# Performance work log

Hardware: AMD Instinct MI355X
Metric: run time of the kernel (lower is better)

Reference implementation:

```python
import jax, jax.numpy as jnp
import numpy as np

DIM, DH, H_HEADS, F, HH, WW = 512, 64, 8, 16, 32, 32
FF_IN = int(DIM * 4 * 2 / 3)  # 1365


def _ln(x, w, b):
    m = x.mean(-1, keepdims=True)
    v = ((x - m) ** 2).mean(-1, keepdims=True)
    return (x - m) * jax.lax.rsqrt(v + 1e-5) * w + b


def _attn(x, ln_w, ln_b, wq, wkv, nkv, nbias, wout, oln_w, oln_b, rel_bias):
    # x: (B, N, D); K/V are single-head (shared across heads) per the source to_kv
    B, N, D = x.shape
    H = nbias.shape[0]
    dh = nkv.shape[-1]
    xn = _ln(x, ln_w, ln_b)
    q = (xn @ wq).reshape(B, N, H, dh).transpose(0, 2, 1, 3) * (dh ** -0.5)
    k, v = jnp.split(xn @ wkv, 2, axis=-1)  # (B, N, dh) each
    nk = jnp.broadcast_to(nkv[0], (B, 1, dh))
    nv = jnp.broadcast_to(nkv[1], (B, 1, dh))
    k = jnp.concatenate([nk, k], axis=1)  # (B, N+1, dh)
    v = jnp.concatenate([nv, v], axis=1)
    sim = jnp.einsum('bhid,bjd->bhij', q, k)  # (B, H, N, N+1)
    bias = jnp.concatenate([jnp.broadcast_to(nbias[:, None, None], (H, N, 1)), rel_bias], axis=-1)
    attn = jax.nn.softmax(sim + bias[None], axis=-1)
    out = jnp.einsum('bhij,bjd->bhid', attn, v)
    out = out.transpose(0, 2, 1, 3).reshape(B, N, H * dh)
    return _ln(out @ wout, oln_w, oln_b)


def _cpb_mlp(coords, w0, b0, w1, b1, w2, b2):
    t = jax.nn.silu(coords @ w0 + b0)
    t = jax.nn.silu(t @ w1 + b1)
    return t @ w2 + b2  # (R, heads)


def _spatial_bias(h, w, w0, b0, w1, b1, w2, b2):
    rh = jnp.arange(-h + 1, h)
    rw = jnp.arange(-w + 1, w)
    gh, gw = jnp.meshgrid(rh, rw, indexing='ij')
    coords = jnp.stack([gh, gw], axis=-1).reshape(-1, 2).astype(jnp.float32)
    table = _cpb_mlp(coords, w0, b0, w1, b1, w2, b2)  # ((2h-1)(2w-1), H)
    ph, pw = jnp.meshgrid(jnp.arange(h), jnp.arange(w), indexing='ij')
    p = jnp.stack([ph, pw], axis=-1).reshape(-1, 2)  # (hw, 2)
    rel = p[:, None] - p[None]  # (hw, hw, 2)
    idx = (rel[..., 0] + h - 1) * (2 * w - 1) + (rel[..., 1] + w - 1)
    return table[idx].transpose(2, 0, 1)  # (H, hw, hw)


def _temporal_bias(f, w0, b0, w1, b1, w2, b2):
    coords = jnp.arange(-f + 1, f, dtype=jnp.float32)[:, None]
    table = _cpb_mlp(coords, w0, b0, w1, b1, w2, b2)  # (2f-1, H)
    idx = jnp.arange(f)[:, None] - jnp.arange(f)[None] + f - 1
    return table[idx].transpose(2, 0, 1)  # (H, f, f)


def _ff(x, win, g, wout):
    # 1x1x1 conv == channel matmul; GEGLU; shift_token; ChanLayerNorm; conv out
    y = jnp.einsum('bcfhw,cd->bdfhw', x, win)
    a, gate = jnp.split(y, 2, axis=1)
    y = a * jax.nn.gelu(gate, approximate=False)
    c = y.shape[1]
    c1 = (c + 1) // 2  # torch.chunk: first chunk gets ceil
    y1, y2 = y[:, :c1], y[:, c1:]
    y2 = jnp.pad(y2, ((0, 0), (0, 0), (1, 0), (0, 0), (0, 0)))[:, :, :-1]
    y = jnp.concatenate([y1, y2], axis=1)
    m = y.mean(1, keepdims=True)
    v = ((y - m) ** 2).mean(1, keepdims=True)
    y = (y - m) * jax.lax.rsqrt(jnp.maximum(v, 1e-5)) * g.reshape(1, -1, 1, 1, 1)
    return jnp.einsum('bcfhw,cd->bdfhw', y, wout)


def setup_inputs() -> dict:
    key = jax.random.key(0)
    ks = jax.random.split(key, 32)
    d2 = DIM // 2
    inner = DH * H_HEADS

    def nrm(k, shape, s=0.02):
        return jax.random.normal(k, shape, jnp.float32) * s

    inp = {'x': jax.random.normal(ks[0], (1, DIM, F, HH, WW), jnp.float32)}
    for pre, i in (('sa', 1), ('ta', 11)):
        inp[pre + '_ln_w'] = jnp.ones(DIM, jnp.float32)
        inp[pre + '_ln_b'] = jnp.zeros(DIM, jnp.float32)
        inp[pre + '_wq'] = nrm(ks[i], (DIM, inner))
        inp[pre + '_wkv'] = nrm(ks[i + 1], (DIM, 2 * DH))
        inp[pre + '_null_kv'] = nrm(ks[i + 2], (2, DH), 1.0)
        inp[pre + '_null_bias'] = nrm(ks[i + 3], (H_HEADS,), 1.0)
        inp[pre + '_wout'] = nrm(ks[i + 4], (inner, DIM))
        inp[pre + '_oln_w'] = jnp.ones(DIM, jnp.float32)
        inp[pre + '_oln_b'] = jnp.zeros(DIM, jnp.float32)
    inp['sp_w0'] = nrm(ks[20], (2, d2), 0.1); inp['sp_b0'] = jnp.zeros(d2, jnp.float32)
    inp['sp_w1'] = nrm(ks[21], (d2, d2), 0.05); inp['sp_b1'] = jnp.zeros(d2, jnp.float32)
    inp['sp_w2'] = nrm(ks[22], (d2, H_HEADS), 0.05); inp['sp_b2'] = jnp.zeros(H_HEADS, jnp.float32)
    inp['tp_w0'] = nrm(ks[23], (1, d2), 0.1); inp['tp_b0'] = jnp.zeros(d2, jnp.float32)
    inp['tp_w1'] = nrm(ks[24], (d2, d2), 0.05); inp['tp_b1'] = jnp.zeros(d2, jnp.float32)
    inp['tp_w2'] = nrm(ks[25], (d2, H_HEADS), 0.05); inp['tp_b2'] = jnp.zeros(H_HEADS, jnp.float32)
    inp['ff_win'] = nrm(ks[26], (DIM, 2 * FF_IN))
    inp['ff_g'] = jnp.ones(FF_IN, jnp.float32)
    inp['ff_wout'] = nrm(ks[27], (FF_IN, DIM))
    return inp


def _forward(x, sa_ln_w, sa_ln_b, sa_wq, sa_wkv, sa_null_kv, sa_null_bias, sa_wout, sa_oln_w, sa_oln_b,
             ta_ln_w, ta_ln_b, ta_wq, ta_wkv, ta_null_kv, ta_null_bias, ta_wout, ta_oln_w, ta_oln_b,
             sp_w0, sp_b0, sp_w1, sp_b1, sp_w2, sp_b2,
             tp_w0, tp_b0, tp_w1, tp_b1, tp_w2, tp_b2,
             ff_win, ff_g, ff_wout):
    b, c, f, h, w = x.shape
    # spatial attention over (h*w) tokens, batched over (b*f)
    xs = x.transpose(0, 2, 3, 4, 1).reshape(b * f, h * w, c)
    sb = _spatial_bias(h, w, sp_w0, sp_b0, sp_w1, sp_b1, sp_w2, sp_b2)
    xs = _attn(xs, sa_ln_w, sa_ln_b, sa_wq, sa_wkv, sa_null_kv, sa_null_bias, sa_wout, sa_oln_w, sa_oln_b, sb) + xs
    xv = xs.reshape(b, f, h, w, c).transpose(0, 4, 1, 2, 3)
    # temporal attention over f tokens, batched over (b*h*w)
    xt = xv.transpose(0, 3, 4, 2, 1).reshape(b * h * w, f, c)
    tb = _temporal_bias(f, tp_w0, tp_b0, tp_w1, tp_b1, tp_w2, tp_b2)
    xt = _attn(xt, ta_ln_w, ta_ln_b, ta_wq, ta_wkv, ta_null_kv, ta_null_bias, ta_wout, ta_oln_w, ta_oln_b, tb) + xt
    xv = xt.reshape(b, h, w, f, c).transpose(0, 4, 3, 1, 2)
    # feed-forward with token shift
    return _ff(xv, ff_win, ff_g, ff_wout) + xv


def reference(x, sa_ln_w, sa_ln_b, sa_wq, sa_wkv, sa_null_kv, sa_null_bias, sa_wout, sa_oln_w, sa_oln_b,
              ta_ln_w, ta_ln_b, ta_wq, ta_wkv, ta_null_kv, ta_null_bias, ta_wout, ta_oln_w, ta_oln_b,
              sp_w0, sp_b0, sp_w1, sp_b1, sp_w2, sp_b2,
              tp_w0, tp_b0, tp_w1, tp_b1, tp_w2, tp_b2,
              ff_win, ff_g, ff_wout):
    return _forward(x, sa_ln_w, sa_ln_b, sa_wq, sa_wkv, sa_null_kv, sa_null_bias, sa_wout, sa_oln_w, sa_oln_b,
                    ta_ln_w, ta_ln_b, ta_wq, ta_wkv, ta_null_kv, ta_null_bias, ta_wout, ta_oln_w, ta_oln_b,
                    sp_w0, sp_b0, sp_w1, sp_b1, sp_w2, sp_b2,
                    tp_w0, tp_b0, tp_w1, tp_b1, tp_w2, tp_b2,
                    ff_win, ff_g, ff_wout)
```

## Files before the change

### kernel.cpp

```cpp
#include <hip/hip_runtime.h>
#include <math.h>

#define TOK 16384
#define DIMC 512
#define FFI 1365
#define CH1 683
#define YSLD 1376
#define KVPAD 1056
#define BSTRIDE 1152
#define MASKB (-30000.f)
#define LOG2E 1.4426950408889634f

typedef unsigned int u32;
typedef unsigned short ushort_t;
typedef __attribute__((ext_vector_type(8))) short bf16x8;
typedef __attribute__((ext_vector_type(4))) float f32x4;

__device__ inline ushort_t f2b(float x) {
    u32 u = __float_as_uint(x);
    u32 r = (u + 0x7fffu + ((u >> 16) & 1u)) >> 16;
    return (ushort_t)r;
}
__device__ inline float b2f(ushort_t u) { return __uint_as_float(((u32)u) << 16); }

__device__ inline float exp2_fast(float x) {
    float r;
    asm("v_exp_f32 %0, %1" : "=v"(r) : "v"(x));
    return r;
}

__device__ inline u32 cvt_pk_bf16(float lo, float hi) {
    u32 r;
    asm("v_cvt_pk_bf16_f32 %0, %1, %2" : "=v"(r) : "v"(lo), "v"(hi));
    return r;
}

__device__ inline void gload_lds16(const void* g, void* l) {
    __builtin_amdgcn_global_load_lds(
        (const __attribute__((address_space(1))) u32*)g,
        (__attribute__((address_space(3))) u32*)l, 16, 0, 0);
}

__device__ inline float gelu_exact(float x) {
    return 0.5f * x * (1.f + erff(x * 0.70710678118654752f));
}

__device__ inline void waitcnt_vm4() {
    asm volatile("s_waitcnt vmcnt(4)" ::: "memory");
    __builtin_amdgcn_sched_barrier(0);
}
__device__ inline void waitcnt_vm0() {
    asm volatile("s_waitcnt vmcnt(0)" ::: "memory");
    __builtin_amdgcn_sched_barrier(0);
}

__global__ __launch_bounds__(256) void cpb_kernel(
    const float* __restrict__ w0, const float* __restrict__ b0,
    const float* __restrict__ w1, const float* __restrict__ b1,
    const float* __restrict__ w2, const float* __restrict__ b2,
    float* __restrict__ table, int mode, int nrows)
{
    __shared__ float t0[16][256];
    __shared__ float t1[16][256];
    int r0 = blockIdx.x * 16;
    int t = threadIdx.x;
    float w0t = w0[t], b0t = b0[t];
    float w0t2 = (mode == 0) ? w0[256 + t] : 0.f;
    #pragma unroll
    for (int rr = 0; rr < 16; ++rr) {
        int r = r0 + rr; if (r >= nrows) r = nrows - 1;
        float c0, c1;
        if (mode == 0) { c0 = (float)(r / 63 - 31); c1 = (float)(r % 63 - 31); }
        else           { c0 = (float)(r - 15);      c1 = 0.f; }
        float a = c0 * w0t + b0t;
        if (mode == 0) a += c1 * w0t2;
        t0[rr][t] = a / (1.f + __expf(-a));
    }
    __syncthreads();
    float b1t = b1[t];
    float acc[16];
    #pragma unroll
    for (int rr = 0; rr < 16; ++rr) acc[rr] = b1t;
    for (int k = 0; k < 256; ++k) {
        float w = w1[k * 256 + t];
        #pragma unroll
        for (int rr = 0; rr < 16; ++rr) acc[rr] += t0[rr][k] * w;
    }
    #pragma unroll
    for (int rr = 0; rr < 16; ++rr) {
        float s = acc[rr];
        t1[rr][t] = s / (1.f + __expf(-s));
    }
    __syncthreads();
    if (t < 128) {
        int rr = t >> 3, oo = t & 7;
        int r = r0 + rr;
        if (r < nrows) {
            float o = b2[oo];
            for (int k = 0; k < 256; ++k) o += t1[rr][k] * w2[k * 8 + oo];
            table[r * 8 + oo] = o;
        }
    }
}

__global__ __launch_bounds__(256) void bias_sp_kernel(
    const float* __restrict__ tab, const float* __restrict__ nullbias,
    ushort_t* __restrict__ out)
{
    int pi = blockIdx.x, h = blockIdx.y;
    int phi = pi >> 5, pwi = pi & 31;
    ushort_t* row = out + ((size_t)h * 1024 + pi) * BSTRIDE;
    for (int c = threadIdx.x; c < BSTRIDE; c += 256) {
        float v;
        if (c == 0) v = nullbias[h];
        else if (c <= 1024) {
            int pj = c - 1;
            int phj = pj >> 5, pwj = pj & 31;
            int idx = (phi - phj + 31) * 63 + (pwi - pwj + 31);
            v = tab[idx * 8 + h];
        } else v = MASKB;
        row[c] = f2b(v * LOG2E);
    }
}

__global__ __launch_bounds__(256) void kvinit_kernel(
    const float* __restrict__ nullkv, ushort_t* __restrict__ KP, ushort_t* __restrict__ VT)
{
    int f = blockIdx.x, t = threadIdx.x;
    for (int e = t; e < 32 * 64; e += 256) {
        int rr = e >> 6, d = e & 63;
        int row = (rr == 0) ? 0 : (1024 + rr);
        KP[((size_t)f * KVPAD + row) * 64 + d] = (rr == 0) ? f2b(nullkv[d]) : (ushort_t)0;
    }
    for (int e = t; e < 64 * 32; e += 256) {
        int d = e >> 5, cc = e & 31;
        int col = (cc == 0) ? 0 : (1024 + cc);
        VT[((size_t)f * 64 + d) * KVPAD + col] = (cc == 0) ? f2b(nullkv[64 + d]) : (ushort_t)0;
    }
}

__global__ __launch_bounds__(256) void wcvt_kernel(
    const float* __restrict__ W, int ldw, int c0,
    ushort_t* __restrict__ Bt, int Kp, int K, int Ncols,
    const float* __restrict__ gv, int Nwrite)
{
    __shared__ float tile[32][33];
    int nb = blockIdx.x * 32, kb = blockIdx.y * 32;
    int tx = threadIdx.x & 31, ty = threadIdx.x >> 5;
    #pragma unroll
    for (int it = 0; it < 4; ++it) {
        int k = kb + ty + it * 8, n = nb + tx;
        float v = (k < K && n < Ncols) ? W[(size_t)k * ldw + c0 + n] : 0.f;
        if (gv && k < K) v *= gv[k];
        tile[ty + it * 8][tx] = v;
    }
    __syncthreads();
    #pragma unroll
    for (int it = 0; it < 4; ++it) {
        int n = nb + ty + it * 8, k = kb + tx;
        if (n < Nwrite && k < Kp) Bt[(size_t)n * Kp + k] = f2b(tile[tx][ty + it * 8]);
    }
}

__global__ __launch_bounds__(256) void transpose_in_kernel(
    const float* __restrict__ x, float* __restrict__ dst)
{
    __shared__ float tile[32][33];
    int t0b = blockIdx.x * 32, c0b = blockIdx.y * 32;
    int tx = threadIdx.x & 31, ty = threadIdx.x >> 5;
    #pragma unroll
    for (int it = 0; it < 4; ++it) {
        int c = ty + it * 8;
        tile[c][tx] = x[(size_t)(c0b + c) * TOK + t0b + tx];
    }
    __syncthreads();
    #pragma unroll
    for (int it = 0; it < 4; ++it) {
        int tr = ty + it * 8;
        dst[(size_t)(t0b + tr) * DIMC + c0b + tx] = tile[tx][tr];
    }
}

__global__ __launch_bounds__(256) void ln_bf16_kernel(
    const float* __restrict__ in, ushort_t* __restrict__ out,
    const float* __restrict__ w, const float* __restrict__ b)
{
    __shared__ float r1[4], r2[4];
    size_t base = (size_t)blockIdx.x * DIMC;
    int t = threadIdx.x;
    float x0 = in[base + t], x1 = in[base + 256 + t];
    float s = x0 + x1, s2 = x0 * x0 + x1 * x1;
    #pragma unroll
    for (int o = 32; o > 0; o >>= 1) { s += __shfl_down(s, o, 64); s2 += __shfl_down(s2, o, 64); }
    if ((t & 63) == 0) { r1[t >> 6] = s; r2[t >> 6] = s2; }
    __syncthreads();
    float mean = (r1[0] + r1[1] + r1[2] + r1[3]) * (1.f / 512.f);
    float ex2  = (r2[0] + r2[1] + r2[2] + r2[3]) * (1.f / 512.f);
    float rstd = rsqrtf(ex2 - mean * mean + 1e-5f);
    out[base + t]       = f2b((x0 - mean) * rstd * w[t] + b[t]);
    out[base + 256 + t] = f2b((x1 - mean) * rstd * w[256 + t] + b[256 + t]);
}

__global__ __launch_bounds__(256) void ln_add_kernel(
    const float* __restrict__ proj, float* __restrict__ io,
    const float* __restrict__ w, const float* __restrict__ b)
{
    __shared__ float r1[4], r2[4];
    size_t base = (size_t)blockIdx.x * DIMC;
    int t = threadIdx.x;
    float x0 = proj[base + t], x1 = proj[base + 256 + t];
    float s = x0 + x1, s2 = x0 * x0 + x1 * x1;
    #pragma unroll
    for (int o = 32; o > 0; o >>= 1) { s += __shfl_down(s, o, 64); s2 += __shfl_down(s2, o, 64); }
    if ((t & 63) == 0) { r1[t >> 6] = s; r2[t >> 6] = s2; }
    __syncthreads();
    float mean = (r1[0] + r1[1] + r1[2] + r1[3]) * (1.f / 512.f);
    float ex2  = (r2[0] + r2[1] + r2[2] + r2[3]) * (1.f / 512.f);
    float rstd = rsqrtf(ex2 - mean * mean + 1e-5f);
    io[base + t]       += (x0 - mean) * rstd * w[t] + b[t];
    io[base + 256 + t] += (x1 - mean) * rstd * w[256 + t] + b[256 + t];
}

__global__ __launch_bounds__(128) void permute0_kernel(
    const float* __restrict__ src, float* __restrict__ dst)
{
    int rd = blockIdx.x;
    int rs = (rd & 15) * 1024 + (rd >> 4);
    ((float4*)(dst + (size_t)rd * DIMC))[threadIdx.x] =
        ((const float4*)(src + (size_t)rs * DIMC))[threadIdx.x];
}

__global__ __launch_bounds__(128) void permute1_dual_kernel(
    const float* __restrict__ src, float* __restrict__ dst, ushort_t* __restrict__ dstb)
{
    int rd = blockIdx.x;
    int rs = (rd & 1023) * 16 + (rd >> 10);
    float4 v = ((const float4*)(src + (size_t)rs * DIMC))[threadIdx.x];
    ((float4*)(dst + (size_t)rd * DIMC))[threadIdx.x] = v;
    u32 lo = (u32)f2b(v.x) | ((u32)f2b(v.y) << 16);
    u32 hi = (u32)f2b(v.z) | ((u32)f2b(v.w) << 16);
    ((uint2*)(dstb + (size_t)rd * DIMC))[threadIdx.x] = make_uint2(lo, hi);
}

template<int EPI>
__global__ __launch_bounds__(256) void gemm_mfma(
    const ushort_t* __restrict__ A, int lda,
    const ushort_t* __restrict__ Bt, int Kp,
    float* __restrict__ C, ushort_t* __restrict__ Cb, int ldc,
    int M, int N, int K, float scale, int nx,
    const float* __restrict__ stats, const float* __restrict__ g,
    const float* __restrict__ resid, float* __restrict__ outT,
    ushort_t* __restrict__ KPo, ushort_t* __restrict__ VTo)
{
    __shared__ __align__(16) ushort_t As[2][4 * 128 * 8];
    __shared__ __align__(16) ushort_t Bs[2][4 * 128 * 8];
    int lin = blockIdx.x;
    int xcd = lin & 7, idx = lin >> 3;
    int m0 = (xcd * 16 + (idx & 15)) * 128;
    int n0 = (idx >> 4) * 128;
    int tid = threadIdx.x, lane = tid & 63, wid = tid >> 6;
    int wy = wid >> 1, wx = wid & 1, quad = lane >> 4, l16 = lane & 15;
    bool bfull = (n0 + 128 <= N);
    f32x4 acc[4][4];
    #pragma unroll
    for (int i = 0; i < 4; ++i)
        #pragma unroll
        for (int j = 0; j < 4; ++j) { acc[i][j][0]=0.f; acc[i][j][1]=0.f; acc[i][j][2]=0.f; acc[i][j][3]=0.f; }

    if (bfull) {
        int NT = K >> 5;
        int c0 = wid * 128 + lane, c1 = wid * 128 + 64 + lane;
        const ushort_t* gA0 = A + (size_t)(m0 + (c0 & 127)) * lda + (c0 >> 7) * 8;
        const ushort_t* gA1 = A + (size_t)(m0 + (c1 & 127)) * lda + (c1 >> 7) * 8;
        const ushort_t* gB0 = Bt + (size_t)(n0 + (c0 & 127)) * Kp + (c0 >> 7) * 8;
        const ushort_t* gB1 = Bt + (size_t)(n0 + (c1 & 127)) * Kp + (c1 >> 7) * 8;
        const int lo0 = (wid * 128) * 8, lo1 = (wid * 128 + 64) * 8;
        auto stage = [&](int buf) {
            gload_lds16(gA0, &As[buf][lo0]);
            gload_lds16(gA1, &As[buf][lo1]);
            gload_lds16(gB0, &Bs[buf][lo0]);
            gload_lds16(gB1, &Bs[buf][lo1]);
            gA0 += 32; gA1 += 32; gB0 += 32; gB1 += 32;
        };
        stage(0);
        if (NT > 1) stage(1);
        for (int t = 0; t < NT; ++t) {
            if (t + 1 < NT) waitcnt_vm4(); else waitcnt_vm0();
            __builtin_amdgcn_s_barrier();
            int cur = t & 1;
            bf16x8 af[4], bfr[4];
            #pragma unroll
            for (int i = 0; i < 4; ++i) af[i] = *(bf16x8*)&As[cur][(quad * 128 + wy * 64 + i * 16 + l16) * 8];
            #pragma unroll
            for (int j = 0; j < 4; ++j) bfr[j] = *(bf16x8*)&Bs[cur][(quad * 128 + wx * 64 + j * 16 + l16) * 8];
            #pragma unroll
            for (int i = 0; i < 4; ++i)
                #pragma unroll
                for (int j = 0; j < 4; ++j)
                    acc[i][j] = __builtin_amdgcn_mfma_f32_16x16x32_bf16(af[i], bfr[j], acc[i][j], 0, 0, 0);
            if (t + 2 < NT) {
                __builtin_amdgcn_s_barrier();
                stage(cur);
            }
        }
    } else {
        for (int k0 = 0; k0 < K; k0 += 32) {
            if (k0) __syncthreads();
            #pragma unroll
            for (int r = 0; r < 2; ++r) {
                int c = wid * 128 + r * 64 + lane;
                const ushort_t* src = A + (size_t)(m0 + (c & 127)) * lda + k0 + (c >> 7) * 8;
                gload_lds16(src, &As[0][(wid * 128 + r * 64) * 8]);
            }
            #pragma unroll
            for (int r = 0; r < 2; ++r) {
                int c = tid + r * 256;
                int kg = c >> 7, nloc = c & 127;
                bf16x8 v;
                if (n0 + nloc < N) v = *(const bf16x8*)(Bt + (size_t)(n0 + nloc) * Kp + k0 + kg * 8);
                else { for (int e = 0; e < 8; ++e) v[e] = 0; }
                *(bf16x8*)&Bs[0][c * 8] = v;
            }
            __syncthreads();
            bf16x8 af[4], bfr[4];
            #pragma unroll
            for (int i = 0; i < 4; ++i) af[i] = *(bf16x8*)&As[0][(quad * 128 + wy * 64 + i * 16 + l16) * 8];
            #pragma unroll
            for (int j = 0; j < 4; ++j) bfr[j] = *(bf16x8*)&Bs[0][(quad * 128 + wx * 64 + j * 16 + l16) * 8];
            #pragma unroll
            for (int i = 0; i < 4; ++i)
                #pragma unroll
                for (int j = 0; j < 4; ++j)
                    acc[i][j] = __builtin_amdgcn_mfma_f32_16x16x32_bf16(af[i], bfr[j], acc[i][j], 0, 0, 0);
        }
    }
    #pragma unroll
    for (int i = 0; i < 4; ++i) {
        #pragma unroll
        for (int j = 0; j < 4; ++j) {
            #pragma unroll
            for (int r = 0; r < 4; ++r) {
                int m = m0 + wy * 64 + i * 16 + quad * 4 + r;
                int n = n0 + wx * 64 + j * 16 + l16;
                if (n >= N) continue;
                float v = acc[i][j][r] * scale;
                if (EPI == 0) {
                    C[(size_t)m * ldc + n] = v;
                } else if (EPI == 3) {
                    Cb[(size_t)m * ldc + n] = f2b(v);
                } else if (EPI == 4) {
                    int frame = m >> 10, tt = m & 1023;
                    if (n < 64) KPo[((size_t)frame * KVPAD + 1 + tt) * 64 + n] = f2b(v);
                    else        VTo[((size_t)frame * 64 + (n - 64)) * KVPAD + 1 + tt] = f2b(v);
                } else if (EPI == 5) {
                    float s0 = stats[2 * m], s1 = stats[2 * m + 1];
                    outT[(size_t)n * TOK + m] = v * s1 - s0 * g[n] + resid[(size_t)m * DIMC + n];
                }
            }
        }
    }
}

__global__ __launch_bounds__(256) void ff_gemm_fused(
    const ushort_t* __restrict__ A,
    const ushort_t* __restrict__ BI,
    ushort_t* __restrict__ YS)
{
    __shared__ __align__(16) ushort_t As[2][4 * 128 * 8];
    __shared__ __align__(16) ushort_t Bs[2][4 * 2 * 64 * 8];
    int lin = blockIdx.x;
    int xcd = lin & 7, idx = lin >> 3;
    int m0 = (xcd * 16 + (idx & 15)) * 128;
    int n0 = (idx >> 4) * 64;
    int tid = threadIdx.x, lane = tid & 63, wid = tid >> 6;
    int wy = wid >> 1, wx = wid & 1, quad = lane >> 4, l16 = lane & 15;
    f32x4 aA[4][2], aG[4][2];
    #pragma unroll
    for (int i = 0; i < 4; ++i)
        #pragma unroll
        for (int j = 0; j < 2; ++j) {
            aA[i][j][0]=0.f; aA[i][j][1]=0.f; aA[i][j][2]=0.f; aA[i][j][3]=0.f;
            aG[i][j][0]=0.f; aG[i][j][1]=0.f; aG[i][j][2]=0.f; aG[i][j][3]=0.f;
        }

    int c0 = wid * 128 + lane, c1 = wid * 128 + 64 + lane;
    const ushort_t* gA0 = A + (size_t)(m0 + (c0 & 127)) * 512 + (c0 >> 7) * 8;
    const ushort_t* gA1 = A + (size_t)(m0 + (c1 & 127)) * 512 + (c1 >> 7) * 8;
    const ushort_t* gB0 = BI + (size_t)((n0 + lane) * 2 + 0) * 512 + wid * 8;
    const ushort_t* gB1 = BI + (size_t)((n0 + lane) * 2 + 1) * 512 + wid * 8;
    const int lo0 = (wid * 128) * 8, lo1 = (wid * 128 + 64) * 8;
    auto stage = [&](int buf) {
        gload_lds16(gA0, &As[buf][lo0]);
        gload_lds16(gA1, &As[buf][lo1]);
        gload_lds16(gB0, &Bs[buf][lo0]);
        gload_lds16(gB1, &Bs[buf][lo1]);
        gA0 += 32; gA1 += 32; gB0 += 32; gB1 += 32;
    };

    stage(0); stage(1);
    for (int t = 0; t < 16; ++t) {
        if (t + 1 < 16) waitcnt_vm4(); else waitcnt_vm0();
        __builtin_amdgcn_s_barrier();
        int cur = t & 1;
        bf16x8 af[4], ba[2], bg[2];
        #pragma unroll
        for (int i = 0; i < 4; ++i) af[i] = *(bf16x8*)&As[cur][(quad * 128 + wy * 64 + i * 16 + l16) * 8];
        #pragma unroll
        for (int j = 0; j < 2; ++j) {
            int nn = wx * 32 + j * 16 + l16;
            ba[j] = *(bf16x8*)&Bs[cur][(quad * 128 + nn) * 8];
            bg[j] = *(bf16x8*)&Bs[cur][(quad * 128 + 64 + nn) * 8];
        }
        #pragma unroll
        for (int i = 0; i < 4; ++i)
            #pragma unroll
            for (int j = 0; j < 2; ++j) {
                aA[i][j] = __builtin_amdgcn_mfma_f32_16x16x32_bf16(af[i], ba[j], aA[i][j], 0, 0, 0);
                aG[i][j] = __builtin_amdgcn_mfma_f32_16x16x32_bf16(af[i], bg[j], aG[i][j], 0, 0, 0);
            }
        if (t + 2 < 16) {
            __builtin_amdgcn_s_barrier();
            stage(cur);
        }
    }
    #pragma unroll
    for (int i = 0; i < 4; ++i) {
        #pragma unroll
        for (int j = 0; j < 2; ++j) {
            #pragma unroll
            for (int r = 0; r < 4; ++r) {
                int m = m0 + wy * 64 + i * 16 + quad * 4 + r;
                int n = n0 + wx * 32 + j * 16 + l16;
                if (n >= FFI) {
                    if (n < YSLD) YS[(size_t)m * YSLD + n] = 0;
                    continue;
                }
                float v = aA[i][j][r] * gelu_exact(aG[i][j][r]);
                int dr = (n < CH1) ? m : m + 1024;
                if (dr < TOK) YS[(size_t)dr * YSLD + n] = f2b(v);
                if (n >= CH1 && m < 1024) YS[(size_t)m * YSLD + n] = 0;
            }
        }
    }
}

__global__ __launch_bounds__(256) void attn_sp_mfma(
    const ushort_t* __restrict__ Q,
    const ushort_t* __restrict__ KP,
    const ushort_t* __restrict__ VT,
    const ushort_t* __restrict__ BIASX,
    ushort_t* __restrict__ O)
{
    __shared__ __align__(16) ushort_t Ks[128 * 64];
    __shared__ __align__(16) ushort_t Vs[64 * 128];
    int lin = blockIdx.x;
    int xcd = lin & 7, idx = lin >> 3;
    int qt = xcd * 8 + (idx & 7);
    int frame = idx >> 3;
    int q0 = qt * 16;
    int tid = threadIdx.x, lane = tid & 63, wid = tid >> 6;
    int quad = lane >> 4, l16 = lane & 15;

    bf16x8 aQ[2][2];
    const ushort_t* brow[2];
    #pragma unroll
    for (int i = 0; i < 2; ++i) {
        int h = wid * 2 + i;
        const ushort_t* qp = Q + (size_t)(frame * 1024 + q0 + l16) * 512 + h * 64 + quad * 8;
        aQ[i][0] = *(const bf16x8*)qp;
        aQ[i][1] = *(const bf16x8*)(qp + 32);
        brow[i] = BIASX + ((size_t)h * 1024 + q0 + l16) * BSTRIDE;
    }
    f32x4 Oc[2][4];
    f32x4 Oc4[2];
    #pragma unroll
    for (int i = 0; i < 2; ++i) {
        #pragma unroll
        for (int nt = 0; nt < 4; ++nt) { Oc[i][nt][0]=0.f; Oc[i][nt][1]=0.f; Oc[i][nt][2]=0.f; Oc[i][nt][3]=0.f; }
        Oc4[i][0]=0.f; Oc4[i][1]=0.f; Oc4[i][2]=0.f; Oc4[i][3]=0.f;
    }
    bf16x8 vones;
    #pragma unroll
    for (int e = 0; e < 8; ++e) vones[e] = (short)0x3F80;

    int idxA = (((quad & 1) * 32) + l16) * 4;
    int idxB = idxA + 64;
    bool hiq = (quad >= 2);

    for (int jt = 0; jt < 9; ++jt) {
        __syncthreads();
        #pragma unroll
        for (int r = 0; r < 4; ++r) {
            int L = wid * 256 + r * 64 + lane;
            int c = L >> 3, gp = L & 7, gg = gp ^ (c & 7);
            int jj = jt * 128 + c; if (jj > KVPAD - 1) jj = KVPAD - 1;
            gload_lds16(KP + ((size_t)frame * KVPAD + jj) * 64 + gg * 8, &Ks[(wid * 256 + r * 64) * 8]);
        }
        #pragma unroll
        for (int r = 0; r < 4; ++r) {
            int L = wid * 256 + r * 64 + lane;
            int d = L >> 4, cgp = L & 15;
            int cg = (cgp & 8) | ((cgp & 7) ^ (d & 7));
            int col = jt * 128 + cg * 8; if (col > KVPAD - 8) col = KVPAD - 8;
            gload_lds16(VT + ((size_t)frame * 64 + d) * KVPAD + col, &Vs[(wid * 256 + r * 64) * 8]);
        }
        __syncthreads();

        #pragma unroll
        for (int i = 0; i < 2; ++i) {
            f32x4 S[8];
            #pragma unroll
            for (int j = 0; j < 8; ++j) { S[j][0]=0.f; S[j][1]=0.f; S[j][2]=0.f; S[j][3]=0.f; }
            __builtin_amdgcn_s_setprio(1);
            #pragma unroll
            for (int j = 0; j < 8; ++j) {
                int c = j * 16 + l16;
                #pragma unroll
                for (int ks = 0; ks < 2; ++ks) {
                    bf16x8 kb = *(bf16x8*)&Ks[(c * 8 + ((ks * 4 + quad) ^ (c & 7))) * 8];
                    S[j] = __builtin_amdgcn_mfma_f32_16x16x32_bf16(kb, aQ[i][ks], S[j], 0, 0, 0);
                }
            }
            __builtin_amdgcn_s_setprio(0);
            #pragma unroll
            for (int j = 0; j < 8; ++j) {
                int kbase = jt * 128 + j * 16 + quad * 4;
                uint2 bv = *(const uint2*)(brow[i] + kbase);
                S[j][0] = exp2_fast(S[j][0] + __uint_as_float(bv.x << 16));
                S[j][1] = exp2_fast(S[j][1] + __uint_as_float(bv.x & 0xffff0000u));
                S[j][2] = exp2_fast(S[j][2] + __uint_as_float(bv.y << 16));
                S[j][3] = exp2_fast(S[j][3] + __uint_as_float(bv.y & 0xffff0000u));
            }
            __builtin_amdgcn_s_setprio(1);
            #pragma unroll
            for (int ks = 0; ks < 4; ++ks) {
                int jl = 2 * ks, jh = 2 * ks + 1;
                u32 pxl = cvt_pk_bf16(S[jl][0], S[jl][1]);
                u32 pyl = cvt_pk_bf16(S[jl][2], S[jl][3]);
                u32 pxh = cvt_pk_bf16(S[jh][0], S[jh][1]);
                u32 pyh = cvt_pk_bf16(S[jh][2], S[jh][3]);
                u32 a0 = (u32)__builtin_amdgcn_ds_bpermute(idxA, (int)pxl);
                u32 a1 = (u32)__builtin_amdgcn_ds_bpermute(idxA, (int)pxh);
                u32 b0 = (u32)__builtin_amdgcn_ds_bpermute(idxA, (int)pyl);
                u32 b1 = (u32)__builtin_amdgcn_ds_bpermute(idxA, (int)pyh);
                u32 c0 = (u32)__builtin_amdgcn_ds_bpermute(idxB, (int)pxl);
                u32 c1 = (u32)__builtin_amdgcn_ds_bpermute(idxB, (int)pxh);
                u32 d0 = (u32)__builtin_amdgcn_ds_bpermute(idxB, (int)pyl);
                u32 d1 = (u32)__builtin_amdgcn_ds_bpermute(idxB, (int)pyh);
                union { u32 w[4]; bf16x8 v; } pa;
                pa.w[0] = hiq ? a1 : a0;
                pa.w[1] = hiq ? b1 : b0;
                pa.w[2] = hiq ? c1 : c0;
                pa.w[3] = hiq ? d1 : d0;
                #pragma unroll
                for (int nt = 0; nt < 4; ++nt) {
                    int d = nt * 16 + l16;
                    int cg = ks * 4 + quad;
                    int phys = (cg & 8) | ((cg & 7) ^ (d & 7));
                    bf16x8 vb = *(bf16x8*)&Vs[(d * 16 + phys) * 8];
                    Oc[i][nt] = __builtin_amdgcn_mfma_f32_16x16x32_bf16(pa.v, vb, Oc[i][nt], 0, 0, 0);
                }
                Oc4[i] = __builtin_amdgcn_mfma_f32_16x16x32_bf16(pa.v, vones, Oc4[i], 0, 0, 0);
            }
            __builtin_amdgcn_s_setprio(0);
        }
    }
    #pragma unroll
    for (int i = 0; i < 2; ++i) {
        int h = wid * 2 + i;
        #pragma unroll
        for (int r = 0; r < 4; ++r) {
            float linv = 1.f / Oc4[i][r];
            int ql = quad * 4 + r;
            #pragma unroll
            for (int nt = 0; nt < 4; ++nt) {
                int d = nt * 16 + l16;
                O[(size_t)(frame * 1024 + q0 + ql) * 512 + h * 64 + d] = f2b(Oc[i][nt][r] * linv);
            }
        }
    }
}

__global__ __launch_bounds__(256) void attn_tp_kernel(
    const ushort_t* __restrict__ q, const ushort_t* __restrict__ kv,
    const float* __restrict__ nullkv, const float* __restrict__ nullbias,
    const float* __restrict__ table, ushort_t* __restrict__ out)
{
    __shared__ float qs[16][512];
    __shared__ float ks[17][64];
    __shared__ float vs[17][64];
    __shared__ float sc[8][16][17];
    int b = blockIdx.x;
    int t = threadIdx.x;
    for (int e = t; e < 16 * 64; e += 256) {
        int f = e >> 6, c8 = e & 63;
        uint4 v = *(const uint4*)(q + (size_t)(b * 16 + f) * 512 + c8 * 8);
        float* dst = &qs[f][c8 * 8];
        dst[0] = b2f((ushort_t)(v.x & 0xffffu)); dst[1] = b2f((ushort_t)(v.x >> 16));
        dst[2] = b2f((ushort_t)(v.y & 0xffffu)); dst[3] = b2f((ushort_t)(v.y >> 16));
        dst[4] = b2f((ushort_t)(v.z & 0xffffu)); dst[5] = b2f((ushort_t)(v.z >> 16));
        dst[6] = b2f((ushort_t)(v.w & 0xffffu)); dst[7] = b2f((ushort_t)(v.w >> 16));
    }
    for (int e = t; e < 17 * 64; e += 256) {
        int j = e >> 6, d = e & 63;
        ks[j][d] = (j == 0) ? nullkv[d]      : b2f(kv[(size_t)(b * 16 + j - 1) * 128 + d]);
        vs[j][d] = (j == 0) ? nullkv[64 + d] : b2f(kv[(size_t)(b * 16 + j - 1) * 128 + 64 + d]);
    }
    __syncthreads();
    for (int e = t; e < 8 * 16 * 17; e += 256) {
        int h = e / 272, rem = e - h * 272;
        int i = rem / 17, j = rem - i * 17;
        float acc = 0.f;
        const float4* qp = (const float4*)&qs[i][h * 64];
        const float4* kp = (const float4*)&ks[j][0];
        #pragma unroll
        for (int d4 = 0; d4 < 16; ++d4) {
            float4 qv = qp[d4], kv4 = kp[d4];
            acc += qv.x * kv4.x;
            acc += qv.y * kv4.y;
            acc += qv.z * kv4.z;
            acc += qv.w * kv4.w;
        }
        float bias = ((j == 0) ? nullbias[h] : table[(i - (j - 1) + 15) * 8 + h]) * LOG2E;
        sc[h][i][j] = acc + bias;
    }
    __syncthreads();
    if (t < 128) {
        int h = t >> 4, i = t & 15;
        float mx = -1e30f;
        for (int j = 0; j < 17; ++j) mx = fmaxf(mx, sc[h][i][j]);
        float s = 0.f;
        for (int j = 0; j < 17; ++j) { float p = exp2_fast(sc[h][i][j] - mx); sc[h][i][j] = p; s += p; }
        float inv = 1.f / s;
        for (int j = 0; j < 17; ++j) sc[h][i][j] *= inv;
    }
    __syncthreads();
    for (int e = t; e < 16 * 128; e += 256) {
        int i = e >> 7, c4 = e & 127;
        int h = c4 >> 4, d4 = c4 & 15;
        float ax = 0.f, ay = 0.f, az = 0.f, aw = 0.f;
        #pragma unroll
        for (int j = 0; j < 17; ++j) {
            float p = sc[h][i][j];
            float4 vv = *(const float4*)&vs[j][d4 * 4];
            ax += p * vv.x; ay += p * vv.y; az += p * vv.z; aw += p * vv.w;
        }
        u32 lo = (u32)f2b(ax) | ((u32)f2b(ay) << 16);
        u32 hi = (u32)f2b(az) | ((u32)f2b(aw) << 16);
        *(uint2*)(out + (size_t)(b * 16 + i) * 512 + c4 * 4) = make_uint2(lo, hi);
    }
}

__global__ __launch_bounds__(256) void rowstats_bf16_kernel(
    const ushort_t* __restrict__ YS, float* __restrict__ stats)
{
    __shared__ float r1[4], r2[4];
    int r = blockIdx.x, t = threadIdx.x;
    const ushort_t* row = YS + (size_t)r * YSLD;
    float s = 0.f, s2 = 0.f;
    for (int c = t; c < FFI; c += 256) {
        float v = b2f(row[c]);
        s += v; s2 += v * v;
    }
    #pragma unroll
    for (int o = 32; o > 0; o >>= 1) { s += __shfl_down(s, o, 64); s2 += __shfl_down(s2, o, 64); }
    if ((t & 63) == 0) { r1[t >> 6] = s; r2[t >> 6] = s2; }
    __syncthreads();
    float S  = r1[0] + r1[1] + r1[2] + r1[3];
    float S2 = r2[0] + r2[1] + r2[2] + r2[3];
    float mean = S * (1.f / 1365.f);
    float var  = S2 * (1.f / 1365.f) - mean * mean;
    float rstd = rsqrtf(fmaxf(var, 1e-5f));
    if (t == 0) { stats[2 * r] = mean * rstd; stats[2 * r + 1] = rstd; }
}

__global__ __launch_bounds__(64) void colsum_kernel(
    const ushort_t* __restrict__ Wt, float* __restrict__ colsum)
{
    int n = blockIdx.x, t = threadIdx.x;
    const ushort_t* row = Wt + (size_t)n * YSLD;
    float s = 0.f;
    for (int k = t; k < YSLD; k += 64) s += b2f(row[k]);
    #pragma unroll
    for (int o = 32; o > 0; o >>= 1) s += __shfl_down(s, o, 64);
    if (t == 0) colsum[n] = s;
}

extern "C" void kernel_launch(void* const* d_in, const int* in_sizes, int n_in,
                              void* d_out, int out_size, void* d_ws, size_t ws_size,
                              hipStream_t stream)
{
    const float* x          = (const float*)d_in[0];
    const float* sa_ln_w    = (const float*)d_in[1];
    const float* sa_ln_b    = (const float*)d_in[2];
    const float* sa_wq      = (const float*)d_in[3];
    const float* sa_wkv     = (const float*)d_in[4];
    const float* sa_null_kv = (const float*)d_in[5];
    const float* sa_null_b  = (const float*)d_in[6];
    const float* sa_wout    = (const float*)d_in[7];
    const float* sa_oln_w   = (const float*)d_in[8];
    const float* sa_oln_b   = (const float*)d_in[9];
    const float* ta_ln_w    = (const float*)d_in[10];
    const float* ta_ln_b    = (const float*)d_in[11];
    const float* ta_wq      = (const float*)d_in[12];
    const float* ta_wkv     = (const float*)d_in[13];
    const float* ta_null_kv = (const float*)d_in[14];
    const float* ta_null_b  = (const float*)d_in[15];
    const float* ta_wout    = (const float*)d_in[16];
    const float* ta_oln_w   = (const float*)d_in[17];
    const float* ta_oln_b   = (const float*)d_in[18];
    const float* sp_w0      = (const float*)d_in[19];
    const float* sp_b0      = (const float*)d_in[20];
    const float* sp_w1      = (const float*)d_in[21];
    const float* sp_b1      = (const float*)d_in[22];
    const float* sp_w2      = (const float*)d_in[23];
    const float* sp_b2      = (const float*)d_in[24];
    const float* tp_w0      = (const float*)d_in[25];
    const float* tp_b0      = (const float*)d_in[26];
    const float* tp_w1      = (const float*)d_in[27];
    const float* tp_b1      = (const float*)d_in[28];
    const float* tp_w2      = (const float*)d_in[29];
    const float* tp_b2      = (const float*)d_in[30];
    const float* ff_win     = (const float*)d_in[31];
    const float* ff_g       = (const float*)d_in[32];
    const float* ff_wout    = (const float*)d_in[33];

    char* ws = (char*)d_ws;
    float*    RES   = (float*)(ws + 0);
    ushort_t* XN16  = (ushort_t*)(ws + 33554432);
    ushort_t* Q16   = (ushort_t*)(ws + 50331648);
    float*    RT    = (float*)(ws + 50331648);
    ushort_t* YS    = (ushort_t*)(ws + 50331648);
    ushort_t* WSA   = (ushort_t*)(ws + 67108864);
    ushort_t* KP    = (ushort_t*)(ws + 83886080);
    ushort_t* VTb   = (ushort_t*)(ws + 86048768);
    ushort_t* KV16  = (ushort_t*)(ws + 83886080);
    ushort_t* WTA   = (ushort_t*)(ws + 90439680);
    ushort_t* AO16  = (ushort_t*)(ws + 92274688);
    ushort_t* BI    = (ushort_t*)(ws + 96468992);
    ushort_t* WFFB  = (ushort_t*)(ws + 99352576);
    ushort_t* BIAS16= (ushort_t*)(ws + 109051904);
    float*    PRJ   = (float*)(ws + 109051904);
    ushort_t* Q16t  = (ushort_t*)(ws + 109051904);
    float*    STATS = (float*)(ws + 142606336);
    float*    SPT   = (float*)(ws + 142737408);
    float*    COLSUM= (float*)(ws + 142737408);
    float*    TPT   = (float*)(ws + 142864448);

    ushort_t* WQ_T  = WSA;
    ushort_t* WKV_T = WSA + 262144;
    ushort_t* WO_T  = WSA + 327680;
    ushort_t* tWQ_T  = WTA;
    ushort_t* tWKV_T = WTA + 262144;
    ushort_t* tWO_T  = WTA + 327680;

    dim3 blk(256);
    const float QSCL = 0.125f * LOG2E;

    cpb_kernel<<<dim3(249), blk, 0, stream>>>(sp_w0, sp_b0, sp_w1, sp_b1, sp_w2, sp_b2, SPT, 0, 3969);
    cpb_kernel<<<dim3(2),   blk, 0, stream>>>(tp_w0, tp_b0, tp_w1, tp_b1, tp_w2, tp_b2, TPT, 1, 31);
    bias_sp_kernel<<<dim3(1024, 8), blk, 0, stream>>>(SPT, sa_null_b, BIAS16);
    kvinit_kernel<<<dim3(16), blk, 0, stream>>>(sa_null_kv, KP, VTb);

    wcvt_kernel<<<dim3(16, 16), blk, 0, stream>>>(sa_wq, 512, 0, WQ_T, 512, 512, 512, nullptr, 512);
    wcvt_kernel<<<dim3(4, 16),  blk, 0, stream>>>(sa_wkv, 128, 0, WKV_T, 512, 512, 128, nullptr, 128);
    wcvt_kernel<<<dim3(16, 16), blk, 0, stream>>>(sa_wout, 512, 0, WO_T, 512, 512, 512, nullptr, 512);
    transpose_in_kernel<<<dim3(512, 16), blk, 0, stream>>>(x, RES);
    ln_bf16_kernel<<<dim3(TOK), blk, 0, stream>>>(RES, XN16, sa_ln_w, sa_ln_b);
    gemm_mfma<3><<<dim3(512), blk, 0, stream>>>(XN16, 512, WQ_T, 512,
        nullptr, Q16, 512, TOK, 512, 512, QSCL, 4, nullptr, nullptr, nullptr, nullptr, nullptr, nullptr);
    gemm_mfma<4><<<dim3(128), blk, 0, stream>>>(XN16, 512, WKV_T, 512,
        nullptr, nullptr, 0, TOK, 128, 512, 1.0f, 1, nullptr, nullptr, nullptr, nullptr, KP, VTb);
    attn_sp_mfma<<<dim3(1024), blk, 0, stream>>>(Q16, KP, VTb, BIAS16, AO16);
    gemm_mfma<0><<<dim3(512), blk, 0, stream>>>(AO16, 512, WO_T, 512,
        PRJ, nullptr, 512, TOK, 512, 512, 1.0f, 4, nullptr, nullptr, nullptr, nullptr, nullptr, nullptr);
    ln_add_kernel<<<dim3(TOK), blk, 0, stream>>>(PRJ, RES, sa_oln_w, sa_oln_b);

    permute0_kernel<<<dim3(TOK), dim3(128), 0, stream>>>(RES, RT);
    wcvt_kernel<<<dim3(16, 16), blk, 0, stream>>>(ta_wq, 512, 0, tWQ_T, 512, 512, 512, nullptr, 512);
    wcvt_kernel<<<dim3(4, 16),  blk, 0, stream>>>(ta_wkv, 128, 0, tWKV_T, 512, 512, 128, nullptr, 128);
    wcvt_kernel<<<dim3(16, 16), blk, 0, stream>>>(ta_wout, 512, 0, tWO_T, 512, 512, 512, nullptr, 512);
    ln_bf16_kernel<<<dim3(TOK), blk, 0, stream>>>(RT, XN16, ta_ln_w, ta_ln_b);
    gemm_mfma<3><<<dim3(512), blk, 0, stream>>>(XN16, 512, tWQ_T, 512,
        nullptr, Q16t, 512, TOK, 512, 512, QSCL, 4, nullptr, nullptr, nullptr, nullptr, nullptr, nullptr);
    gemm_mfma<3><<<dim3(128), blk, 0, stream>>>(XN16, 512, tWKV_T, 512,
        nullptr, KV16, 128, TOK, 128, 512, 1.0f, 1, nullptr, nullptr, nullptr, nullptr, nullptr, nullptr);
    attn_tp_kernel<<<dim3(1024), blk, 0, stream>>>(Q16t, KV16, ta_null_kv, ta_null_b, TPT, AO16);
    gemm_mfma<0><<<dim3(512), blk, 0, stream>>>(AO16, 512, tWO_T, 512,
        PRJ, nullptr, 512, TOK, 512, 512, 1.0f, 4, nullptr, nullptr, nullptr, nullptr, nullptr, nullptr);
    ln_add_kernel<<<dim3(TOK), blk, 0, stream>>>(PRJ, RT, ta_oln_w, ta_oln_b);
    permute1_dual_kernel<<<dim3(TOK), dim3(128), 0, stream>>>(RT, RES, XN16);

    wcvt_kernel<<<dim3(44, 16), blk, 0, stream>>>(ff_win, 2730, 0,   BI,       1024, 512, FFI, nullptr, 1408);
    wcvt_kernel<<<dim3(44, 16), blk, 0, stream>>>(ff_win, 2730, FFI, BI + 512, 1024, 512, FFI, nullptr, 1408);
    wcvt_kernel<<<dim3(16, 43), blk, 0, stream>>>(ff_wout, 512, 0, WFFB, YSLD, FFI, 512, ff_g, 512);
    colsum_kernel<<<dim3(512), dim3(64), 0, stream>>>(WFFB, COLSUM);
    ff_gemm_fused<<<dim3(2816), blk, 0, stream>>>(XN16, BI, YS);
    rowstats_bf16_kernel<<<dim3(TOK), blk, 0, stream>>>(YS, STATS);
    gemm_mfma<5><<<dim3(512), blk, 0, stream>>>(YS, YSLD, WFFB, YSLD,
        nullptr, nullptr, 0, TOK, 512, YSLD, 1.0f, 4, STATS, COLSUM, RES, (float*)d_out, nullptr, nullptr);
}
```

Before: 855.5 us.

## Process two query tiles per block in spatial attention to reuse K/V loads

The spatial attention kernel now handles 32 query rows per block (two 16-row sub-tiles) instead of 16, halving the grid to 512 blocks. Each K/V tile staged in shared memory is therefore reused for twice as many queries, which cuts global-to-LDS traffic and barrier count per unit of work. In exchange each thread holds twice the accumulators and Q fragments, raising register pressure and possibly lowering occupancy, and the smaller grid may underfill the GPU. Separately, the temporal attention kernel pads its shared-memory arrays to avoid bank conflicts.

```diff
diff --git a/kernel.cpp b/kernel.cpp
--- a/kernel.cpp
+++ b/kernel.cpp
@@ -455,30 +455,35 @@
     __shared__ __align__(16) ushort_t Vs[64 * 128];
     int lin = blockIdx.x;
     int xcd = lin & 7, idx = lin >> 3;
-    int qt = xcd * 8 + (idx & 7);
-    int frame = idx >> 3;
-    int q0 = qt * 16;
+    int qp = idx & 3;
+    int frame = idx >> 2;
+    int q0 = xcd * 128 + qp * 32;
     int tid = threadIdx.x, lane = tid & 63, wid = tid >> 6;
     int quad = lane >> 4, l16 = lane & 15;
 
-    bf16x8 aQ[2][2];
-    const ushort_t* brow[2];
+    bf16x8 aQ[2][2][2];
+    const ushort_t* brow[2][2];
     #pragma unroll
     for (int i = 0; i < 2; ++i) {
         int h = wid * 2 + i;
-        const ushort_t* qp = Q + (size_t)(frame * 1024 + q0 + l16) * 512 + h * 64 + quad * 8;
-        aQ[i][0] = *(const bf16x8*)qp;
-        aQ[i][1] = *(const bf16x8*)(qp + 32);
-        brow[i] = BIASX + ((size_t)h * 1024 + q0 + l16) * BSTRIDE;
-    }
-    f32x4 Oc[2][4];
-    f32x4 Oc4[2];
-    #pragma unroll
-    for (int i = 0; i < 2; ++i) {
-        #pragma unroll
-        for (int nt = 0; nt < 4; ++nt) { Oc[i][nt][0]=0.f; Oc[i][nt][1]=0.f; Oc[i][nt][2]=0.f; Oc[i][nt][3]=0.f; }
-        Oc4[i][0]=0.f; Oc4[i][1]=0.f; Oc4[i][2]=0.f; Oc4[i][3]=0.f;
-    }
+        #pragma unroll
+        for (int qq = 0; qq < 2; ++qq) {
+            const ushort_t* qptr = Q + (size_t)(frame * 1024 + q0 + qq * 16 + l16) * 512 + h * 64 + quad * 8;
+            aQ[i][qq][0] = *(const bf16x8*)qptr;
+            aQ[i][qq][1] = *(const bf16x8*)(qptr + 32);
+            brow[i][qq] = BIASX + ((size_t)h * 1024 + q0 + qq * 16 + l16) * BSTRIDE;
+        }
+    }
+    f32x4 Oc[2][2][4];
+    f32x4 Oc4[2][2];
+    #pragma unroll
+    for (int i = 0; i < 2; ++i)
+        #pragma unroll
+        for (int qq = 0; qq < 2; ++qq) {
+            #pragma unroll
+            for (int nt = 0; nt < 4; ++nt) { Oc[i][qq][nt][0]=0.f; Oc[i][qq][nt][1]=0.f; Oc[i][qq][nt][2]=0.f; Oc[i][qq][nt][3]=0.f; }
+            Oc4[i][qq][0]=0.f; Oc4[i][qq][1]=0.f; Oc4[i][qq][2]=0.f; Oc4[i][qq][3]=0.f;
+        }
     bf16x8 vones;
     #pragma unroll
     for (int e = 0; e < 8; ++e) vones[e] = (short)0x3F80;
@@ -508,74 +513,80 @@
 
         #pragma unroll
         for (int i = 0; i < 2; ++i) {
-            f32x4 S[8];
-            #pragma unroll
-            for (int j = 0; j < 8; ++j) { S[j][0]=0.f; S[j][1]=0.f; S[j][2]=0.f; S[j][3]=0.f; }
-            __builtin_amdgcn_s_setprio(1);
-            #pragma unroll
-            for (int j = 0; j < 8; ++j) {
-                int c = j * 16 + l16;
+            #pragma unroll
+            for (int qq = 0; qq < 2; ++qq) {
+                f32x4 S[8];
                 #pragma unroll
-                for (int ks = 0; ks < 2; ++ks) {
-                    bf16x8 kb = *(bf16x8*)&Ks[(c * 8 + ((ks * 4 + quad) ^ (c & 7))) * 8];
-                    S[j] = __builtin_amdgcn_mfma_f32_16x16x32_bf16(kb, aQ[i][ks], S[j], 0, 0, 0);
+                for (int j = 0; j < 8; ++j) { S[j][0]=0.f; S[j][1]=0.f; S[j][2]=0.f; S[j][3]=0.f; }
+                __builtin_amdgcn_s_setprio(1);
+                #pragma unroll
+                for (int j = 0; j < 8; ++j) {
+                    int c = j * 16 + l16;
+                    #pragma unroll
+                    for (int ks = 0; ks < 2; ++ks) {
+                        bf16x8 kb = *(bf16x8*)&Ks[(c * 8 + ((ks * 4 + quad) ^ (c & 7))) * 8];
+                        S[j] = __builtin_amdgcn_mfma_f32_16x16x32_bf16(kb, aQ[i][qq][ks], S[j], 0, 0, 0);
+                    }
                 }
+                __builtin_amdgcn_s_setprio(0);
+                #pragma unroll
+                for (int j = 0; j < 8; ++j) {
+                    int kbase = jt * 128 + j * 16 + quad * 4;
+                    uint2 bv = *(const uint2*)(brow[i][qq] + kbase);
+                    S[j][0] = exp2_fast(S[j][0] + __uint_as_float(bv.x << 16));
+                    S[j][1] = exp2_fast(S[j][1] + __uint_as_float(bv.x & 0xffff0000u));
+                    S[j][2] = exp2_fast(S[j][2] + __uint_as_float(bv.y << 16));
+                    S[j][3] = exp2_fast(S[j][3] + __uint_as_float(bv.y & 0xffff0000u));
+                }
+                __builtin_amdgcn_s_setprio(1);
+                #pragma unroll
+                for (int ks = 0; ks < 4; ++ks) {
+                    int jl = 2 * ks, jh = 2 * ks + 1;
+                    u32 pxl = cvt_pk_bf16(S[jl][0], S[jl][1]);
+                    u32 pyl = cvt_pk_bf16(S[jl][2], S[jl][3]);
+                    u32 pxh = cvt_pk_bf16(S[jh][0], S[jh][1]);
+                    u32 pyh = cvt_pk_bf16(S[jh][2], S[jh][3]);
+                    u32 a0 = (u32)__builtin_amdgcn_ds_bpermute(idxA, (int)pxl);
+                    u32 a1 = (u32)__builtin_amdgcn_ds_bpermute(idxA, (int)pxh);
+                    u32 b0 = (u32)__builtin_amdgcn_ds_bpermute(idxA, (int)pyl);
+                    u32 b1 = (u32)__builtin_amdgcn_ds_bpermute(idxA, (int)pyh);
+                    u32 c0 = (u32)__builtin_amdgcn_ds_bpermute(idxB, (int)pxl);
+                    u32 c1 = (u32)__builtin_amdgcn_ds_bpermute(idxB, (int)pxh);
+                    u32 d0 = (u32)__builtin_amdgcn_ds_bpermute(idxB, (int)pyl);
+                    u32 d1 = (u32)__builtin_amdgcn_ds_bpermute(idxB, (int)pyh);
+                    union { u32 w[4]; bf16x8 v; } pa;
+                    pa.w[0] = hiq ? a1 : a0;
+                    pa.w[1] = hiq ? b1 : b0;
+                    pa.w[2] = hiq ? c1 : c0;
+                    pa.w[3] = hiq ? d1 : d0;
+                    #pragma unroll
+                    for (int nt = 0; nt < 4; ++nt) {
+                        int d = nt * 16 + l16;
+                        int cg = ks * 4 + quad;
+                        int phys = (cg & 8) | ((cg & 7) ^ (d & 7));
+                        bf16x8 vb = *(bf16x8*)&Vs[(d * 16 + phys) * 8];
+                        Oc[i][qq][nt] = __builtin_amdgcn_mfma_f32_16x16x32_bf16(pa.v, vb, Oc[i][qq][nt], 0, 0, 0);
+                    }
+                    Oc4[i][qq] = __builtin_amdgcn_mfma_f32_16x16x32_bf16(pa.v, vones, Oc4[i][qq], 0, 0, 0);
+                }
+                __builtin_amdgcn_s_setprio(0);
             }
-            __builtin_amdgcn_s_setprio(0);
-            #pragma unroll
-            for (int j = 0; j < 8; ++j) {
-                int kbase = jt * 128 + j * 16 + quad * 4;
-                uint2 bv = *(const uint2*)(brow[i] + kbase);
-                S[j][0] = exp2_fast(S[j][0] + __uint_as_float(bv.x << 16));
-                S[j][1] = exp2_fast(S[j][1] + __uint_as_float(bv.x & 0xffff0000u));
-                S[j][2] = exp2_fast(S[j][2] + __uint_as_float(bv.y << 16));
-                S[j][3] = exp2_fast(S[j][3] + __uint_as_float(bv.y & 0xffff0000u));
-            }
-            __builtin_amdgcn_s_setprio(1);
-            #pragma unroll
-            for (int ks = 0; ks < 4; ++ks) {
-                int jl = 2 * ks, jh = 2 * ks + 1;
-                u32 pxl = cvt_pk_bf16(S[jl][0], S[jl][1]);
-                u32 pyl = cvt_pk_bf16(S[jl][2], S[jl][3]);
-                u32 pxh = cvt_pk_bf16(S[jh][0], S[jh][1]);
-                u32 pyh = cvt_pk_bf16(S[jh][2], S[jh][3]);
-                u32 a0 = (u32)__builtin_amdgcn_ds_bpermute(idxA, (int)pxl);
-                u32 a1 = (u32)__builtin_amdgcn_ds_bpermute(idxA, (int)pxh);
-                u32 b0 = (u32)__builtin_amdgcn_ds_bpermute(idxA, (int)pyl);
-                u32 b1 = (u32)__builtin_amdgcn_ds_bpermute(idxA, (int)pyh);
-                u32 c0 = (u32)__builtin_amdgcn_ds_bpermute(idxB, (int)pxl);
-                u32 c1 = (u32)__builtin_amdgcn_ds_bpermute(idxB, (int)pxh);
-                u32 d0 = (u32)__builtin_amdgcn_ds_bpermute(idxB, (int)pyl);
-                u32 d1 = (u32)__builtin_amdgcn_ds_bpermute(idxB, (int)pyh);
-                union { u32 w[4]; bf16x8 v; } pa;
-                pa.w[0] = hiq ? a1 : a0;
-                pa.w[1] = hiq ? b1 : b0;
-                pa.w[2] = hiq ? c1 : c0;
-                pa.w[3] = hiq ? d1 : d0;
+        }
+    }
+    #pragma unroll
+    for (int i = 0; i < 2; ++i) {
+        int h = wid * 2 + i;
+        #pragma unroll
+        for (int qq = 0; qq < 2; ++qq) {
+            #pragma unroll
+            for (int r = 0; r < 4; ++r) {
+                float linv = 1.f / Oc4[i][qq][r];
+                int ql = qq * 16 + quad * 4 + r;
                 #pragma unroll
                 for (int nt = 0; nt < 4; ++nt) {
                     int d = nt * 16 + l16;
-                    int cg = ks * 4 + quad;
-                    int phys = (cg & 8) | ((cg & 7) ^ (d & 7));
-                    bf16x8 vb = *(bf16x8*)&Vs[(d * 16 + phys) * 8];
-                    Oc[i][nt] = __builtin_amdgcn_mfma_f32_16x16x32_bf16(pa.v, vb, Oc[i][nt], 0, 0, 0);
+                    O[(size_t)(frame * 1024 + q0 + ql) * 512 + h * 64 + d] = f2b(Oc[i][qq][nt][r] * linv);
                 }
-                Oc4[i] = __builtin_amdgcn_mfma_f32_16x16x32_bf16(pa.v, vones, Oc4[i], 0, 0, 0);
-            }
-            __builtin_amdgcn_s_setprio(0);
-        }
-    }
-    #pragma unroll
-    for (int i = 0; i < 2; ++i) {
-        int h = wid * 2 + i;
-        #pragma unroll
-        for (int r = 0; r < 4; ++r) {
-            float linv = 1.f / Oc4[i][r];
-            int ql = quad * 4 + r;
-            #pragma unroll
-            for (int nt = 0; nt < 4; ++nt) {
-                int d = nt * 16 + l16;
-                O[(size_t)(frame * 1024 + q0 + ql) * 512 + h * 64 + d] = f2b(Oc[i][nt][r] * linv);
             }
         }
     }
@@ -586,9 +597,9 @@
     const float* __restrict__ nullkv, const float* __restrict__ nullbias,
     const float* __restrict__ table, ushort_t* __restrict__ out)
 {
-    __shared__ float qs[16][512];
-    __shared__ float ks[17][64];
-    __shared__ float vs[17][64];
+    __shared__ float qs[16][516];
+    __shared__ float ks[17][68];
+    __shared__ float vs[17][68];
     __shared__ float sc[8][16][17];
     int b = blockIdx.x;
     int t = threadIdx.x;
@@ -771,7 +782,7 @@
         nullptr, Q16, 512, TOK, 512, 512, QSCL, 4, nullptr, nullptr, nullptr, nullptr, nullptr, nullptr);
     gemm_mfma<4><<<dim3(128), blk, 0, stream>>>(XN16, 512, WKV_T, 512,
         nullptr, nullptr, 0, TOK, 128, 512, 1.0f, 1, nullptr, nullptr, nullptr, nullptr, KP, VTb);
-    attn_sp_mfma<<<dim3(1024), blk, 0, stream>>>(Q16, KP, VTb, BIAS16, AO16);
+    attn_sp_mfma<<<dim3(512), blk, 0, stream>>>(Q16, KP, VTb, BIAS16, AO16);
     gemm_mfma<0><<<dim3(512), blk, 0, stream>>>(AO16, 512, WO_T, 512,
         PRJ, nullptr, 512, TOK, 512, 512, 1.0f, 4, nullptr, nullptr, nullptr, nullptr, nullptr, nullptr);
     ln_add_kernel<<<dim3(TOK), blk, 0, stream>>>(PRJ, RES, sa_oln_w, sa_oln_b);
```

After: 832.7 us. 2.7% less time.
